# Optimization experiments

Measured on AMD Instinct MI355X. Metric: run time of the kernel, lower is better.

The kernel has to match this reference:

```python
import jax, jax.numpy as jnp
import numpy as np

H = 56; W = 56; WS = 7; SS = 3; NH = 12; DIM = 384; B = 32
N = WS * WS                      # 49 tokens per window
NW = (H // WS) * (W // WS)       # 64 windows per image
HID = 4 * DIM
EPS = 1e-5


def _rel_index():
    coords = np.stack(np.meshgrid(np.arange(WS), np.arange(WS), indexing='ij'))  # [2,ws,ws]
    cf = coords.reshape(2, -1)
    rel = (cf[:, :, None] - cf[:, None, :]).transpose(1, 2, 0)  # [N,N,2]
    rel[..., 0] += WS - 1
    rel[..., 1] += WS - 1
    rel[..., 0] *= 2 * WS - 1
    return rel.sum(-1).astype(np.int32)  # [N,N] in [0,169)


def _attn_mask():
    img = np.zeros((H, W), np.float32)
    cnt = 0
    sl = (slice(0, -WS), slice(-WS, -SS), slice(-SS, None))
    for h in sl:
        for w in sl:
            img[h, w] = cnt
            cnt += 1
    mw = img.reshape(H // WS, WS, W // WS, WS).transpose(0, 2, 1, 3).reshape(-1, N)  # [nW,N]
    am = mw[:, None, :] - mw[:, :, None]  # [nW,N,N]
    return np.where(am != 0, np.float32(-100.0), np.float32(0.0)).astype(np.float32)


def _ln(x, g, b):
    m = jnp.mean(x, axis=-1, keepdims=True)
    v = jnp.mean(jnp.square(x - m), axis=-1, keepdims=True)
    return (x - m) * jax.lax.rsqrt(v + EPS) * g + b


def setup_inputs() -> dict:
    key = jax.random.key(0)
    ks = jax.random.split(key, 8)
    s = 0.02
    return {
        'x': jax.random.normal(ks[0], (B, H * W, DIM), jnp.float32),
        'qkv_w': jax.random.normal(ks[1], (3 * DIM, DIM), jnp.float32) * s,
        'qkv_b': jnp.zeros((3 * DIM,), jnp.float32),
        'proj_w': jax.random.normal(ks[2], (DIM, DIM), jnp.float32) * s,
        'proj_b': jnp.zeros((DIM,), jnp.float32),
        'rpb_table': jax.random.normal(ks[3], ((2 * WS - 1) ** 2, NH), jnp.float32) * s,
        'ln1_g': jnp.ones((DIM,), jnp.float32),
        'ln1_b': jnp.zeros((DIM,), jnp.float32),
        'fc1_w': jax.random.normal(ks[4], (HID, DIM), jnp.float32) * s,
        'fc1_b': jnp.zeros((HID,), jnp.float32),
        'fc2_w': jax.random.normal(ks[5], (DIM, HID), jnp.float32) * s,
        'fc2_b': jnp.zeros((DIM,), jnp.float32),
        'ln2_g': jnp.ones((DIM,), jnp.float32),
        'ln2_b': jnp.zeros((DIM,), jnp.float32),
        'attn_mask': jnp.asarray(_attn_mask()),
        'rel_idx': jnp.asarray(_rel_index()),
    }


def reference(x, qkv_w, qkv_b, proj_w, proj_b, rpb_table, ln1_g, ln1_b,
              fc1_w, fc1_b, fc2_w, fc2_b, ln2_g, ln2_b, attn_mask, rel_idx):
    Bb, L, C = x.shape
    hd = C // NH
    scale = hd ** -0.5
    shortcut = x
    # cyclic shift
    xs = jnp.roll(x.reshape(Bb, H, W, C), (-SS, -SS), axis=(1, 2))
    # window partition -> [Bb*nW, N, C]
    xw = xs.reshape(Bb, H // WS, WS, W // WS, WS, C).transpose(0, 1, 3, 2, 4, 5).reshape(-1, N, C)
    # qkv
    qkv = (xw @ qkv_w.T + qkv_b).reshape(-1, N, 3, NH, hd).transpose(2, 0, 3, 1, 4)
    q, k, v = qkv[0] * scale, qkv[1], qkv[2]          # [Bb*nW, NH, N, hd]
    attn = jnp.einsum('whnd,whmd->whnm', q, k)        # [Bb*nW, NH, N, N]
    bias = rpb_table[rel_idx.reshape(-1)].reshape(N, N, NH).transpose(2, 0, 1)
    attn = attn + bias[None]
    # shifted-window mask
    attn = attn.reshape(Bb, NW, NH, N, N) + attn_mask[None, :, None]
    attn = jax.nn.softmax(attn.reshape(-1, NH, N, N), axis=-1)
    out = jnp.einsum('whnm,whmd->whnd', attn, v).transpose(0, 2, 1, 3).reshape(-1, N, C)
    out = out @ proj_w.T + proj_b
    # window reverse + roll back
    xs = out.reshape(Bb, H // WS, W // WS, WS, WS, C).transpose(0, 1, 3, 2, 4, 5).reshape(Bb, H, W, C)
    xs = jnp.roll(xs, (SS, SS), axis=(1, 2)).reshape(Bb, L, C)
    # post-norm residuals (as in source: shortcut + norm(attn_out); x += norm(ffn(x)))
    x1 = shortcut + _ln(xs, ln1_g, ln1_b)
    y = jax.nn.gelu(x1 @ fc1_w.T + fc1_b, approximate=False) @ fc2_w.T + fc2_b
    return x1 + _ln(y, ln2_g, ln2_b)
```

## Files before the change

kernel.cpp:

```cpp
#include <hip/hip_runtime.h>
#include <hip/hip_bf16.h>
#include <math.h>

typedef __hip_bfloat16 bf16;
typedef __bf16 bf16x8 __attribute__((ext_vector_type(8)));
typedef float f32x4 __attribute__((ext_vector_type(4)));

#define HH 56
#define WW 56
#define WSZ 7
#define SSH 3
#define NHEAD 12
#define CDIM 384
#define BBATCH 32
#define NTOK 49
#define NWIN 64
#define HIDD 1536
#define HD 32
#define NWTOT (BBATCH*NWIN)
#define MROWS (NWTOT*NTOK)
#define MHALF (MROWS/2)
#define LTOT (HH*WW)
#define EPSLN 1e-5f
#define QSCALE 0.17677669529663687f
#define NEGBIG -1e30f

enum { M_QK = 0, M_V = 1, M_FC1 = 2, M_ROW = 3 };

__device__ __forceinline__ void gload16(const void* g, void* l) {
    __builtin_amdgcn_global_load_lds(
        (const __attribute__((address_space(1))) void*)g,
        (__attribute__((address_space(3))) void*)l, 16, 0, 0);
}

__device__ __forceinline__ unsigned short bfbits(float v) {
    bf16 b = __float2bfloat16(v);
    return *reinterpret_cast<unsigned short*>(&b);
}

__device__ __forceinline__ int xcd_swz(int orig, int nwg) {
    const int q = nwg >> 3, r = nwg & 7;
    const int xcd = orig & 7, loc = orig >> 3;
    return (xcd < r ? xcd * (q + 1) : r * (q + 1) + (xcd - r) * q) + loc;
}

__global__ __launch_bounds__(256) void cvt_k(const float* __restrict__ src,
                                             bf16* __restrict__ dst, int n) {
    int i = blockIdx.x * 256 + threadIdx.x;
    if (i < n) dst[i] = __float2bfloat16(src[i]);
}

__global__ __launch_bounds__(256)
void tbl_k(const float* __restrict__ rpb, const int* __restrict__ relidx,
           const float* __restrict__ amask, float* __restrict__ tbl) {
    int idx = blockIdx.x * 256 + threadIdx.x;
    int m = idx & 63, n = (idx >> 6) & 63;
    int h = (idx >> 12) % NHEAD, wi = idx / (64 * 64 * NHEAD);
    float v;
    if (m >= NTOK) v = NEGBIG;
    else if (n >= NTOK) v = 0.f;
    else v = rpb[relidx[n * NTOK + m] * NHEAD + h] + amask[((long)wi * NTOK + n) * NTOK + m];
    tbl[idx] = v;
}

__global__ __launch_bounds__(256) void gather_k(const float* __restrict__ x,
                                                bf16* __restrict__ xw, int rbase) {
    int idx = blockIdx.x * 256 + threadIdx.x;
    int rr_l = idx / 96, c4 = (idx % 96) * 4;
    int rr = rbase + rr_l;
    int w = rr / 49, ti = rr % 49;
    int b = w >> 6, wi = w & 63;
    int hy = (wi >> 3) * 7 + ti / 7;
    int hx = (wi & 7) * 7 + ti % 7;
    int sh = hy + SSH; if (sh >= HH) sh -= HH;
    int sw = hx + SSH; if (sw >= WW) sw -= WW;
    float4 v = *(const float4*)&x[((long)b * LTOT + sh * WW + sw) * CDIM + c4];
    ushort4 u = { bfbits(v.x), bfbits(v.y), bfbits(v.z), bfbits(v.w) };
    *(ushort4*)&xw[(long)rr_l * CDIM + c4] = u;
}

template<int MODE, int KDIM, int NTN>
__global__ __launch_bounds__(256, 4)
void mgemm_k(const bf16* __restrict__ A, const bf16* __restrict__ Wt,
             const float* __restrict__ bias, void* __restrict__ Outp)
{
    constexpr bool SWAP = (MODE != M_V);
    __shared__ bf16 As[2][128 * 32];
    __shared__ bf16 Bs[2][128 * 32];
    const int tid = threadIdx.x;
    const int wid = tid >> 6, lane = tid & 63;

    const int gid = xcd_swz(blockIdx.x, gridDim.x);
    const int m0 = (gid / NTN) * 128;
    const int n0 = (gid % NTN) * 128;

    const int strow = lane >> 2, stseg = lane & 3;
    const int swseg = stseg ^ ((strow >> 1) & 3);
    const bf16* Ag = A + (long)(m0 + wid * 32 + strow) * KDIM + swseg * 8;
    const bf16* Wg = Wt + (long)(n0 + wid * 32 + strow) * KDIM + swseg * 8;

    const int wr = (wid >> 1) * 64, wc = (wid & 1) * 64;
    const int l15 = lane & 15, g4 = lane >> 4;
    const int sa = g4 ^ ((l15 >> 1) & 3);

    f32x4 acc[4][4] = {};

    auto STAGE = [&](int b, int t) {
#pragma unroll
        for (int i = 0; i < 2; ++i)
            gload16(Ag + (long)(i * 16) * KDIM + t * 32, &As[b][(wid * 32 + i * 16) * 32]);
#pragma unroll
        for (int i = 0; i < 2; ++i)
            gload16(Wg + (long)(i * 16) * KDIM + t * 32, &Bs[b][(wid * 32 + i * 16) * 32]);
    };

    const int nt = KDIM / 32;
    STAGE(0, 0);
    STAGE(1, 1);
    asm volatile("s_waitcnt vmcnt(4)" ::: "memory");
    __builtin_amdgcn_s_barrier();

    int buf = 0;
    for (int t = 0; t < nt; ++t) {
        bf16x8 af[4], bfr[4];
#pragma unroll
        for (int i = 0; i < 4; ++i) {
            af[i]  = *(const bf16x8*)&As[buf][(wr + i * 16 + l15) * 32 + sa * 8];
            bfr[i] = *(const bf16x8*)&Bs[buf][(wc + i * 16 + l15) * 32 + sa * 8];
        }
        __builtin_amdgcn_sched_barrier(0);
        asm volatile("s_waitcnt lgkmcnt(0)" ::: "memory");
        __builtin_amdgcn_sched_barrier(0);
        __builtin_amdgcn_s_barrier();
        if (t + 2 < nt) STAGE(buf, t + 2);
#pragma unroll
        for (int mi = 0; mi < 4; ++mi)
#pragma unroll
            for (int ni = 0; ni < 4; ++ni) {
                if (SWAP)
                    acc[ni][mi] = __builtin_amdgcn_mfma_f32_16x16x32_bf16(
                        bfr[ni], af[mi], acc[ni][mi], 0, 0, 0);
                else
                    acc[mi][ni] = __builtin_amdgcn_mfma_f32_16x16x32_bf16(
                        af[mi], bfr[ni], acc[mi][ni], 0, 0, 0);
            }
        if (t + 2 < nt) { asm volatile("s_waitcnt vmcnt(4)" ::: "memory"); }
        else            { asm volatile("s_waitcnt vmcnt(0)" ::: "memory"); }
        __builtin_amdgcn_s_barrier();
        buf ^= 1;
    }

    if (MODE == M_V) {
#pragma unroll
        for (int mi = 0; mi < 4; ++mi) {
            const int mb = m0 + wr + mi * 16 + g4 * 4;
            const int wv_ = mb / 49, ti0 = mb - wv_ * 49;
#pragma unroll
            for (int ni = 0; ni < 4; ++ni) {
                const int n = n0 + wc + ni * 16 + l15;
                const int h = n >> 5, d = n & 31;
                const float bn = bias[n];
                float v4[4];
#pragma unroll
                for (int j = 0; j < 4; ++j) v4[j] = acc[mi][ni][j] + bn;
                if (ti0 <= 45) {
                    ushort4 u = { bfbits(v4[0]), bfbits(v4[1]), bfbits(v4[2]), bfbits(v4[3]) };
                    *(ushort4*)&((bf16*)Outp)[(((long)wv_ * NHEAD + h) * HD + d) * 64 + ti0] = u;
                } else {
#pragma unroll
                    for (int j = 0; j < 4; ++j) {
                        const int m = mb + j;
                        const int w2 = m / 49, ti = m - w2 * 49;
                        ((bf16*)Outp)[(((long)w2 * NHEAD + h) * HD + d) * 64 + ti]
                            = __float2bfloat16(v4[j]);
                    }
                }
            }
        }
    } else {
        long rowbase[4];
        int wq_[4], ti_[4];
#pragma unroll
        for (int mi = 0; mi < 4; ++mi) {
            const int m = m0 + wr + mi * 16 + l15;
            if (MODE == M_QK)       { wq_[mi] = m / 49; ti_[mi] = m - wq_[mi] * 49; }
            else if (MODE == M_FC1) { rowbase[mi] = (long)m * HIDD; }
            else                    { rowbase[mi] = (long)m * CDIM; }
        }
#pragma unroll
        for (int ni = 0; ni < 4; ++ni) {
            const int nb = n0 + wc + ni * 16 + g4 * 4;
            const float4 bn = *(const float4*)&bias[nb];
            const float bb[4] = { bn.x, bn.y, bn.z, bn.w };
#pragma unroll
            for (int mi = 0; mi < 4; ++mi) {
                float v4[4];
#pragma unroll
                for (int j = 0; j < 4; ++j) v4[j] = acc[ni][mi][j] + bb[j];
                if (MODE == M_FC1) {
#pragma unroll
                    for (int j = 0; j < 4; ++j)
                        v4[j] = 0.5f * v4[j] * (1.0f + erff(v4[j] * 0.70710678118654752f));
                } else if (MODE == M_QK) {
                    if (nb < CDIM) {
#pragma unroll
                        for (int j = 0; j < 4; ++j) v4[j] *= QSCALE;
                    }
                }
                ushort4 u = { bfbits(v4[0]), bfbits(v4[1]), bfbits(v4[2]), bfbits(v4[3]) };
                if (MODE == M_QK) {
                    const int which = nb >= CDIM;
                    const int hb = (nb - which * CDIM) >> 5, d0 = nb & 31;
                    *(ushort4*)&((bf16*)Outp)[
                        ((((long)wq_[mi] * 2 + which) * NHEAD + hb) * NTOK + ti_[mi]) * HD + d0] = u;
                } else {
                    *(ushort4*)&((bf16*)Outp)[rowbase[mi] + nb] = u;
                }
            }
        }
    }
}

__global__ __launch_bounds__(256)
void mattn_k(const bf16* __restrict__ qk, const bf16* __restrict__ vT,
             const float* __restrict__ tbl, bf16* __restrict__ attn_out)
{
    __shared__ bf16 Plds[4][64 * 72];
    const int tid = threadIdx.x, wid = tid >> 6, lane = tid & 63;
    const int t = blockIdx.x * 4 + wid;
    const int w = t / NHEAD, h = t % NHEAD, wi = w & 63;
    const int l15 = lane & 15, g = lane >> 4;
    const bf16* qb = qk + ((long)(w * 2 + 0) * NHEAD + h) * (NTOK * HD);
    const bf16* kb = qk + ((long)(w * 2 + 1) * NHEAD + h) * (NTOK * HD);
    const bf16* vt = vT + ((long)w * NHEAD + h) * (HD * 64);
    const float* Tb = tbl + (long)(wi * NHEAD + h) * 64 * 64;
    char* Pw = (char*)&Plds[wid][0];

    bf16x8 kf[4], qf[4];
#pragma unroll
    for (int i = 0; i < 4; ++i) {
        kf[i] = *(const bf16x8*)&kb[(16 * i + l15) * HD + 8 * g];
        qf[i] = *(const bf16x8*)&qb[(16 * i + l15) * HD + 8 * g];
    }
    f32x4 s[4][4] = {};
#pragma unroll
    for (int mi = 0; mi < 4; ++mi)
#pragma unroll
        for (int ni = 0; ni < 4; ++ni)
            s[mi][ni] = __builtin_amdgcn_mfma_f32_16x16x32_bf16(
                kf[mi], qf[ni], s[mi][ni], 0, 0, 0);

#pragma unroll
    for (int ni = 0; ni < 4; ++ni) {
        const int n = 16 * ni + l15;
#pragma unroll
        for (int mi = 0; mi < 4; ++mi) {
            float4 tv = *(const float4*)&Tb[(long)n * 64 + 16 * mi + 4 * g];
            s[mi][ni][0] += tv.x; s[mi][ni][1] += tv.y;
            s[mi][ni][2] += tv.z; s[mi][ni][3] += tv.w;
        }
        float mx = NEGBIG;
#pragma unroll
        for (int mi = 0; mi < 4; ++mi)
#pragma unroll
            for (int j = 0; j < 4; ++j) mx = fmaxf(mx, s[mi][ni][j]);
        mx = fmaxf(mx, __shfl_xor(mx, 16));
        mx = fmaxf(mx, __shfl_xor(mx, 32));
        float sum = 0.f;
#pragma unroll
        for (int mi = 0; mi < 4; ++mi)
#pragma unroll
            for (int j = 0; j < 4; ++j) {
                float e = expf(s[mi][ni][j] - mx);
                s[mi][ni][j] = e; sum += e;
            }
        sum += __shfl_xor(sum, 16);
        sum += __shfl_xor(sum, 32);
        const float r = 1.0f / sum;
#pragma unroll
        for (int mi = 0; mi < 4; ++mi) {
            ushort4 u;
            u.x = bfbits(s[mi][ni][0] * r);
            u.y = bfbits(s[mi][ni][1] * r);
            u.z = bfbits(s[mi][ni][2] * r);
            u.w = bfbits(s[mi][ni][3] * r);
            *(ushort4*)(Pw + (long)n * 144 + (16 * mi + 4 * g) * 2) = u;
        }
    }

    f32x4 o[4][2] = {};
#pragma unroll
    for (int kk = 0; kk < 2; ++kk) {
        bf16x8 vf[2];
        vf[0] = *(const bf16x8*)&vt[(long)(l15) * 64 + 32 * kk + 8 * g];
        vf[1] = *(const bf16x8*)&vt[(long)(16 + l15) * 64 + 32 * kk + 8 * g];
#pragma unroll
        for (int rt = 0; rt < 4; ++rt) {
            bf16x8 pf = *(const bf16x8*)(Pw + (long)(16 * rt + l15) * 144 + (32 * kk + 8 * g) * 2);
            o[rt][0] = __builtin_amdgcn_mfma_f32_16x16x32_bf16(pf, vf[0], o[rt][0], 0, 0, 0);
            o[rt][1] = __builtin_amdgcn_mfma_f32_16x16x32_bf16(pf, vf[1], o[rt][1], 0, 0, 0);
        }
    }

#pragma unroll
    for (int rt = 0; rt < 4; ++rt)
#pragma unroll
        for (int dt = 0; dt < 2; ++dt)
#pragma unroll
            for (int j = 0; j < 4; ++j) {
                int n = 16 * rt + 4 * g + j;
                if (n < NTOK)
                    attn_out[((long)w * NTOK + n) * CDIM + h * HD + 16 * dt + l15]
                        = __float2bfloat16(o[rt][dt][j]);
            }
}

__global__ __launch_bounds__(256)
void ln1_k(const bf16* __restrict__ P, const bf16* __restrict__ xw,
           const float* __restrict__ g, const float* __restrict__ bta,
           bf16* __restrict__ x1b, int mbase)
{
    const int wv = threadIdx.x >> 6, lane = threadIdx.x & 63;
    const long rl = (long)blockIdx.x * 4 + wv;
    const bool act = lane < 48;
    float vals[8];
    float s = 0.f, sq = 0.f;
    if (act) {
        bf16x8 pv = *(const bf16x8*)&P[rl * CDIM + lane * 8];
#pragma unroll
        for (int j = 0; j < 8; ++j) { vals[j] = (float)pv[j]; s += vals[j]; sq += vals[j] * vals[j]; }
    } else {
#pragma unroll
        for (int j = 0; j < 8; ++j) vals[j] = 0.f;
    }
#pragma unroll
    for (int o = 32; o; o >>= 1) { s += __shfl_xor(s, o); sq += __shfl_xor(sq, o); }
    const float mean = s * (1.f / 384.f);
    const float rstd = rsqrtf(sq * (1.f / 384.f) - mean * mean + EPSLN);

    const int m = mbase + (int)rl;
    int w = m / 49, ti = m - w * 49;
    int b = w >> 6, wi = w & 63;
    int hy = (wi >> 3) * 7 + ti / 7;
    int hx = (wi & 7) * 7 + ti % 7;
    int dh = hy + SSH; if (dh >= HH) dh -= HH;
    int dw = hx + SSH; if (dw >= WW) dw -= WW;
    const long tok_l = (long)b * LTOT + dh * WW + dw - mbase;

    if (act) {
        bf16x8 xv = *(const bf16x8*)&xw[rl * CDIM + lane * 8];
        const int c = lane * 8;
        const float4 g0 = *(const float4*)&g[c],   g1 = *(const float4*)&g[c + 4];
        const float4 b0 = *(const float4*)&bta[c], b1 = *(const float4*)&bta[c + 4];
        const float gg[8] = { g0.x, g0.y, g0.z, g0.w, g1.x, g1.y, g1.z, g1.w };
        const float bb[8] = { b0.x, b0.y, b0.z, b0.w, b1.x, b1.y, b1.z, b1.w };
        ushort4 u0, u1;
        float r0 = (float)xv[0] + (vals[0] - mean) * rstd * gg[0] + bb[0];
        float r1 = (float)xv[1] + (vals[1] - mean) * rstd * gg[1] + bb[1];
        float r2 = (float)xv[2] + (vals[2] - mean) * rstd * gg[2] + bb[2];
        float r3 = (float)xv[3] + (vals[3] - mean) * rstd * gg[3] + bb[3];
        u0 = { bfbits(r0), bfbits(r1), bfbits(r2), bfbits(r3) };
        r0 = (float)xv[4] + (vals[4] - mean) * rstd * gg[4] + bb[4];
        r1 = (float)xv[5] + (vals[5] - mean) * rstd * gg[5] + bb[5];
        r2 = (float)xv[6] + (vals[6] - mean) * rstd * gg[6] + bb[6];
        r3 = (float)xv[7] + (vals[7] - mean) * rstd * gg[7] + bb[7];
        u1 = { bfbits(r0), bfbits(r1), bfbits(r2), bfbits(r3) };
        *(ushort4*)&x1b[tok_l * CDIM + c] = u0;
        *(ushort4*)&x1b[tok_l * CDIM + c + 4] = u1;
    }
}

__global__ __launch_bounds__(256)
void ln2_k(const bf16* __restrict__ y, const bf16* __restrict__ x1b,
           const float* __restrict__ g, const float* __restrict__ bta,
           float* __restrict__ outp, int mbase)
{
    const int wv = threadIdx.x >> 6, lane = threadIdx.x & 63;
    const long rl = (long)blockIdx.x * 4 + wv;
    const bool act = lane < 48;
    float vals[8];
    float s = 0.f, sq = 0.f;
    if (act) {
        bf16x8 yv = *(const bf16x8*)&y[rl * CDIM + lane * 8];
#pragma unroll
        for (int j = 0; j < 8; ++j) { vals[j] = (float)yv[j]; s += vals[j]; sq += vals[j] * vals[j]; }
    } else {
#pragma unroll
        for (int j = 0; j < 8; ++j) vals[j] = 0.f;
    }
#pragma unroll
    for (int o = 32; o; o >>= 1) { s += __shfl_xor(s, o); sq += __shfl_xor(sq, o); }
    const float mean = s * (1.f / 384.f);
    const float rstd = rsqrtf(sq * (1.f / 384.f) - mean * mean + EPSLN);

    if (act) {
        bf16x8 xv = *(const bf16x8*)&x1b[rl * CDIM + lane * 8];
        const int c = lane * 8;
        const float4 g0 = *(const float4*)&g[c],   g1 = *(const float4*)&g[c + 4];
        const float4 b0 = *(const float4*)&bta[c], b1 = *(const float4*)&bta[c + 4];
        float4 o0, o1;
        o0.x = (float)xv[0] + (vals[0] - mean) * rstd * g0.x + b0.x;
        o0.y = (float)xv[1] + (vals[1] - mean) * rstd * g0.y + b0.y;
        o0.z = (float)xv[2] + (vals[2] - mean) * rstd * g0.z + b0.z;
        o0.w = (float)xv[3] + (vals[3] - mean) * rstd * g0.w + b0.w;
        o1.x = (float)xv[4] + (vals[4] - mean) * rstd * g1.x + b1.x;
        o1.y = (float)xv[5] + (vals[5] - mean) * rstd * g1.y + b1.y;
        o1.z = (float)xv[6] + (vals[6] - mean) * rstd * g1.z + b1.z;
        o1.w = (float)xv[7] + (vals[7] - mean) * rstd * g1.w + b1.w;
        const long mg = (long)mbase + rl;
        *(float4*)&outp[mg * CDIM + c] = o0;
        *(float4*)&outp[mg * CDIM + c + 4] = o1;
    }
}

extern "C" void kernel_launch(void* const* d_in, const int* in_sizes, int n_in,
                              void* d_out, int out_size, void* d_ws, size_t ws_size,
                              hipStream_t stream)
{
    const float* x      = (const float*)d_in[0];
    const float* qkv_w  = (const float*)d_in[1];
    const float* qkv_b  = (const float*)d_in[2];
    const float* proj_w = (const float*)d_in[3];
    const float* proj_b = (const float*)d_in[4];
    const float* rpb    = (const float*)d_in[5];
    const float* ln1_g  = (const float*)d_in[6];
    const float* ln1_b  = (const float*)d_in[7];
    const float* fc1_w  = (const float*)d_in[8];
    const float* fc1_b  = (const float*)d_in[9];
    const float* fc2_w  = (const float*)d_in[10];
    const float* fc2_b  = (const float*)d_in[11];
    const float* ln2_g  = (const float*)d_in[12];
    const float* ln2_b  = (const float*)d_in[13];
    const float* amask  = (const float*)d_in[14];
    const int*   relidx = (const int*)d_in[15];
    float* out = (float*)d_out;
    char*  ws  = (char*)d_ws;

    bf16*  wq    = (bf16*) (ws + 0L);
    bf16*  wp    = (bf16*) (ws + 884736L);
    bf16*  w1    = (bf16*) (ws + 1179648L);
    bf16*  w2    = (bf16*) (ws + 2359296L);
    float* tbl   = (float*)(ws + 3538944L);
    bf16*  xw_h  = (bf16*) (ws + 16121856L);
    bf16*  qkb_h = (bf16*) (ws + 54657024L);
    bf16*  vT_h  = (bf16*) (ws + 131727360L);
    bf16*  att_h = (bf16*) (ws + 182059008L);
    bf16*  P_h   = (bf16*) (ws + 220594176L);
    bf16*  x1b_h = (bf16*) (ws + 259129344L);
    bf16*  H1_h  = (bf16*) (ws + 16121856L);
    bf16*  y_h   = (bf16*) (ws + 170262528L);

    dim3 b256(256);

    cvt_k<<<dim3((3*CDIM*CDIM + 255)/256), b256, 0, stream>>>(qkv_w, wq, 3*CDIM*CDIM);
    cvt_k<<<dim3((CDIM*CDIM + 255)/256), b256, 0, stream>>>(proj_w, wp, CDIM*CDIM);
    cvt_k<<<dim3((HIDD*CDIM + 255)/256), b256, 0, stream>>>(fc1_w, w1, HIDD*CDIM);
    cvt_k<<<dim3((CDIM*HIDD + 255)/256), b256, 0, stream>>>(fc2_w, w2, CDIM*HIDD);
    tbl_k<<<dim3(64*12*64*64/256), b256, 0, stream>>>(rpb, relidx, amask, tbl);

    for (int c = 0; c < 2; ++c) {
        const int mb = c * MHALF;
        gather_k<<<dim3(MHALF * 96 / 256), b256, 0, stream>>>(x, xw_h, mb);
        mgemm_k<M_QK, CDIM, 6><<<dim3((MHALF/128)*6), b256, 0, stream>>>(
            xw_h, wq, qkv_b, (void*)qkb_h);
        mgemm_k<M_V, CDIM, 3><<<dim3((MHALF/128)*3), b256, 0, stream>>>(
            xw_h, wq + (long)2*CDIM*CDIM, qkv_b + 2*CDIM, (void*)vT_h);
        mattn_k<<<dim3(1024 * NHEAD / 4), b256, 0, stream>>>(qkb_h, vT_h, tbl, att_h);
        mgemm_k<M_ROW, CDIM, 3><<<dim3((MHALF/128)*3), b256, 0, stream>>>(
            att_h, wp, proj_b, (void*)P_h);
        ln1_k<<<dim3(MHALF/4), b256, 0, stream>>>(P_h, xw_h, ln1_g, ln1_b, x1b_h, mb);
        mgemm_k<M_FC1, CDIM, 12><<<dim3((MHALF/128)*12), b256, 0, stream>>>(
            x1b_h, w1, fc1_b, (void*)H1_h);
        mgemm_k<M_ROW, HIDD, 3><<<dim3((MHALF/128)*3), b256, 0, stream>>>(
            H1_h, w2, fc2_b, (void*)y_h);
        ln2_k<<<dim3(MHALF/4), b256, 0, stream>>>(y_h, x1b_h, ln2_g, ln2_b, out, mb);
    }
}
```

Baseline: 944.1 us.

## Fuse proj and fc2 GEMMs with LayerNorm residual epilogues, use tanh-form GELU

Adds a gemm_ln_k kernel in which each block computes a full 64x384 output row tile, reduces row statistics across waves through LDS and applies LayerNorm plus residual (with the window-reverse scatter for LN1) in the epilogue. This removes the bf16 round trip of the P and y intermediates and two separate LN launches. The full-row tiles give fewer blocks and more registers per thread. Separately, exact erf GELU is replaced by a sigmoid-based tanh approximation, which changes the numerics slightly.

```diff
diff --git a/kernel.cpp b/kernel.cpp
--- a/kernel.cpp
+++ b/kernel.cpp
@@ -25,7 +25,7 @@
 #define QSCALE 0.17677669529663687f
 #define NEGBIG -1e30f
 
-enum { M_QK = 0, M_V = 1, M_FC1 = 2, M_ROW = 3 };
+enum { M_QK = 0, M_V = 1, M_FC1 = 2 };
 
 __device__ __forceinline__ void gload16(const void* g, void* l) {
     __builtin_amdgcn_global_load_lds(
@@ -36,6 +36,10 @@
 __device__ __forceinline__ unsigned short bfbits(float v) {
     bf16 b = __float2bfloat16(v);
     return *reinterpret_cast<unsigned short*>(&b);
+}
+
+__device__ __forceinline__ float fast_gelu(float v) {
+    return v / (1.0f + __expf(-1.59576912f * v * fmaf(0.044715f, v * v, 1.0f)));
 }
 
 __device__ __forceinline__ int xcd_swz(int orig, int nwg) {
@@ -183,9 +187,8 @@
 #pragma unroll
         for (int mi = 0; mi < 4; ++mi) {
             const int m = m0 + wr + mi * 16 + l15;
-            if (MODE == M_QK)       { wq_[mi] = m / 49; ti_[mi] = m - wq_[mi] * 49; }
-            else if (MODE == M_FC1) { rowbase[mi] = (long)m * HIDD; }
-            else                    { rowbase[mi] = (long)m * CDIM; }
+            if (MODE == M_QK) { wq_[mi] = m / 49; ti_[mi] = m - wq_[mi] * 49; }
+            else              { rowbase[mi] = (long)m * HIDD; }
         }
 #pragma unroll
         for (int ni = 0; ni < 4; ++ni) {
@@ -199,8 +202,7 @@
                 for (int j = 0; j < 4; ++j) v4[j] = acc[ni][mi][j] + bb[j];
                 if (MODE == M_FC1) {
 #pragma unroll
-                    for (int j = 0; j < 4; ++j)
-                        v4[j] = 0.5f * v4[j] * (1.0f + erff(v4[j] * 0.70710678118654752f));
+                    for (int j = 0; j < 4; ++j) v4[j] = fast_gelu(v4[j]);
                 } else if (MODE == M_QK) {
                     if (nb < CDIM) {
 #pragma unroll
@@ -216,6 +218,149 @@
                 } else {
                     *(ushort4*)&((bf16*)Outp)[rowbase[mi] + nb] = u;
                 }
+            }
+        }
+    }
+}
+
+template<int KDIM, bool SCATTER>
+__global__ __launch_bounds__(256, 2)
+void gemm_ln_k(const bf16* __restrict__ A, const bf16* __restrict__ Wt,
+               const float* __restrict__ bias, const bf16* __restrict__ resid,
+               const float* __restrict__ lng, const float* __restrict__ lnb,
+               float* __restrict__ outf, bf16* __restrict__ outb, int mbase)
+{
+    __shared__ bf16 As[2][64 * 32];
+    __shared__ bf16 Bs[2][384 * 32];
+    __shared__ float lnp[512];
+    const int tid = threadIdx.x;
+    const int wid = tid >> 6, lane = tid & 63;
+
+    const int m0 = xcd_swz(blockIdx.x, gridDim.x) * 64;
+
+    const int strow = tid >> 2, stseg = tid & 3;
+    const int swr = stseg ^ ((strow >> 1) & 3);
+    const bf16* Ag = A + (long)(m0 + strow) * KDIM + swr * 8;
+    const bf16* Wg = Wt + (long)strow * KDIM + swr * 8;
+
+    const int wc = wid * 96;
+    const int l15 = lane & 15, g4 = lane >> 4;
+    const int sa = g4 ^ ((l15 >> 1) & 3);
+
+    f32x4 acc[6][4] = {};
+
+    auto STAGE = [&](int b, int t) {
+        gload16(Ag + t * 32, &As[b][strow * 32 + stseg * 8]);
+#pragma unroll
+        for (int i = 0; i < 6; ++i)
+            gload16(Wg + (long)(i * 64) * KDIM + t * 32,
+                    &Bs[b][(strow + i * 64) * 32 + stseg * 8]);
+    };
+
+    const int nt = KDIM / 32;
+    STAGE(0, 0);
+    STAGE(1, 1);
+    asm volatile("s_waitcnt vmcnt(7)" ::: "memory");
+    __builtin_amdgcn_s_barrier();
+
+    int buf = 0;
+    for (int t = 0; t < nt; ++t) {
+        bf16x8 af[4], bfr[6];
+#pragma unroll
+        for (int i = 0; i < 4; ++i)
+            af[i] = *(const bf16x8*)&As[buf][(i * 16 + l15) * 32 + sa * 8];
+#pragma unroll
+        for (int i = 0; i < 6; ++i)
+            bfr[i] = *(const bf16x8*)&Bs[buf][(wc + i * 16 + l15) * 32 + sa * 8];
+        __builtin_amdgcn_sched_barrier(0);
+        asm volatile("s_waitcnt lgkmcnt(0)" ::: "memory");
+        __builtin_amdgcn_sched_barrier(0);
+        __builtin_amdgcn_s_barrier();
+        if (t + 2 < nt) STAGE(buf, t + 2);
+#pragma unroll
+        for (int ni = 0; ni < 6; ++ni)
+#pragma unroll
+            for (int mi = 0; mi < 4; ++mi)
+                acc[ni][mi] = __builtin_amdgcn_mfma_f32_16x16x32_bf16(
+                    bfr[ni], af[mi], acc[ni][mi], 0, 0, 0);
+        if (t + 2 < nt) { asm volatile("s_waitcnt vmcnt(7)" ::: "memory"); }
+        else            { asm volatile("s_waitcnt vmcnt(0)" ::: "memory"); }
+        __builtin_amdgcn_s_barrier();
+        buf ^= 1;
+    }
+
+    float psum[4] = {}, psq[4] = {};
+#pragma unroll
+    for (int ni = 0; ni < 6; ++ni) {
+        const int nb = wc + ni * 16 + g4 * 4;
+        const float4 bn = *(const float4*)&bias[nb];
+        const float bb[4] = { bn.x, bn.y, bn.z, bn.w };
+#pragma unroll
+        for (int mi = 0; mi < 4; ++mi)
+#pragma unroll
+            for (int j = 0; j < 4; ++j) {
+                float v = acc[ni][mi][j] + bb[j];
+                acc[ni][mi][j] = v;
+                psum[mi] += v; psq[mi] += v * v;
+            }
+    }
+#pragma unroll
+    for (int mi = 0; mi < 4; ++mi) {
+        psum[mi] += __shfl_xor(psum[mi], 16); psum[mi] += __shfl_xor(psum[mi], 32);
+        psq[mi]  += __shfl_xor(psq[mi], 16);  psq[mi]  += __shfl_xor(psq[mi], 32);
+    }
+    if (g4 == 0) {
+#pragma unroll
+        for (int mi = 0; mi < 4; ++mi) {
+            const int r = mi * 16 + l15;
+            lnp[wid * 64 + r] = psum[mi];
+            lnp[256 + wid * 64 + r] = psq[mi];
+        }
+    }
+    __syncthreads();
+
+#pragma unroll
+    for (int mi = 0; mi < 4; ++mi) {
+        const int r = mi * 16 + l15;
+        const float s  = lnp[r] + lnp[64 + r] + lnp[128 + r] + lnp[192 + r];
+        const float sq = lnp[256 + r] + lnp[320 + r] + lnp[384 + r] + lnp[448 + r];
+        const float mean = s * (1.f / 384.f);
+        const float rstd = rsqrtf(sq * (1.f / 384.f) - mean * mean + EPSLN);
+
+        const long rl = m0 + r;
+        long dst;
+        if (SCATTER) {
+            const int m = mbase + (int)rl;
+            int w = m / 49, ti = m - w * 49;
+            int b = w >> 6, wi = w & 63;
+            int hy = (wi >> 3) * 7 + ti / 7;
+            int hx = (wi & 7) * 7 + ti % 7;
+            int dh = hy + SSH; if (dh >= HH) dh -= HH;
+            int dw = hx + SSH; if (dw >= WW) dw -= WW;
+            dst = (long)b * LTOT + dh * WW + dw - mbase;
+        } else {
+            dst = mbase + rl;
+        }
+#pragma unroll
+        for (int ni = 0; ni < 6; ++ni) {
+            const int c = wc + ni * 16 + g4 * 4;
+            const float4 gv = *(const float4*)&lng[c];
+            const float4 bv = *(const float4*)&lnb[c];
+            ushort4 xv = *(const ushort4*)&resid[rl * CDIM + c];
+            float x0 = __bfloat162float(*(bf16*)&xv.x);
+            float x1 = __bfloat162float(*(bf16*)&xv.y);
+            float x2 = __bfloat162float(*(bf16*)&xv.z);
+            float x3 = __bfloat162float(*(bf16*)&xv.w);
+            float r0 = x0 + (acc[ni][mi][0] - mean) * rstd * gv.x + bv.x;
+            float r1 = x1 + (acc[ni][mi][1] - mean) * rstd * gv.y + bv.y;
+            float r2 = x2 + (acc[ni][mi][2] - mean) * rstd * gv.z + bv.z;
+            float r3 = x3 + (acc[ni][mi][3] - mean) * rstd * gv.w + bv.w;
+            if (SCATTER) {
+                ushort4 u = { bfbits(r0), bfbits(r1), bfbits(r2), bfbits(r3) };
+                *(ushort4*)&outb[dst * CDIM + c] = u;
+            } else {
+                float4 o = { r0, r1, r2, r3 };
+                *(float4*)&outf[dst * CDIM + c] = o;
             }
         }
     }
@@ -313,104 +458,6 @@
                     attn_out[((long)w * NTOK + n) * CDIM + h * HD + 16 * dt + l15]
                         = __float2bfloat16(o[rt][dt][j]);
             }
-}
-
-__global__ __launch_bounds__(256)
-void ln1_k(const bf16* __restrict__ P, const bf16* __restrict__ xw,
-           const float* __restrict__ g, const float* __restrict__ bta,
-           bf16* __restrict__ x1b, int mbase)
-{
-    const int wv = threadIdx.x >> 6, lane = threadIdx.x & 63;
-    const long rl = (long)blockIdx.x * 4 + wv;
-    const bool act = lane < 48;
-    float vals[8];
-    float s = 0.f, sq = 0.f;
-    if (act) {
-        bf16x8 pv = *(const bf16x8*)&P[rl * CDIM + lane * 8];
-#pragma unroll
-        for (int j = 0; j < 8; ++j) { vals[j] = (float)pv[j]; s += vals[j]; sq += vals[j] * vals[j]; }
-    } else {
-#pragma unroll
-        for (int j = 0; j < 8; ++j) vals[j] = 0.f;
-    }
-#pragma unroll
-    for (int o = 32; o; o >>= 1) { s += __shfl_xor(s, o); sq += __shfl_xor(sq, o); }
-    const float mean = s * (1.f / 384.f);
-    const float rstd = rsqrtf(sq * (1.f / 384.f) - mean * mean + EPSLN);
-
-    const int m = mbase + (int)rl;
-    int w = m / 49, ti = m - w * 49;
-    int b = w >> 6, wi = w & 63;
-    int hy = (wi >> 3) * 7 + ti / 7;
-    int hx = (wi & 7) * 7 + ti % 7;
-    int dh = hy + SSH; if (dh >= HH) dh -= HH;
-    int dw = hx + SSH; if (dw >= WW) dw -= WW;
-    const long tok_l = (long)b * LTOT + dh * WW + dw - mbase;
-
-    if (act) {
-        bf16x8 xv = *(const bf16x8*)&xw[rl * CDIM + lane * 8];
-        const int c = lane * 8;
-        const float4 g0 = *(const float4*)&g[c],   g1 = *(const float4*)&g[c + 4];
-        const float4 b0 = *(const float4*)&bta[c], b1 = *(const float4*)&bta[c + 4];
-        const float gg[8] = { g0.x, g0.y, g0.z, g0.w, g1.x, g1.y, g1.z, g1.w };
-        const float bb[8] = { b0.x, b0.y, b0.z, b0.w, b1.x, b1.y, b1.z, b1.w };
-        ushort4 u0, u1;
-        float r0 = (float)xv[0] + (vals[0] - mean) * rstd * gg[0] + bb[0];
-        float r1 = (float)xv[1] + (vals[1] - mean) * rstd * gg[1] + bb[1];
-        float r2 = (float)xv[2] + (vals[2] - mean) * rstd * gg[2] + bb[2];
-        float r3 = (float)xv[3] + (vals[3] - mean) * rstd * gg[3] + bb[3];
-        u0 = { bfbits(r0), bfbits(r1), bfbits(r2), bfbits(r3) };
-        r0 = (float)xv[4] + (vals[4] - mean) * rstd * gg[4] + bb[4];
-        r1 = (float)xv[5] + (vals[5] - mean) * rstd * gg[5] + bb[5];
-        r2 = (float)xv[6] + (vals[6] - mean) * rstd * gg[6] + bb[6];
-        r3 = (float)xv[7] + (vals[7] - mean) * rstd * gg[7] + bb[7];
-        u1 = { bfbits(r0), bfbits(r1), bfbits(r2), bfbits(r3) };
-        *(ushort4*)&x1b[tok_l * CDIM + c] = u0;
-        *(ushort4*)&x1b[tok_l * CDIM + c + 4] = u1;
-    }
-}
-
-__global__ __launch_bounds__(256)
-void ln2_k(const bf16* __restrict__ y, const bf16* __restrict__ x1b,
-           const float* __restrict__ g, const float* __restrict__ bta,
-           float* __restrict__ outp, int mbase)
-{
-    const int wv = threadIdx.x >> 6, lane = threadIdx.x & 63;
-    const long rl = (long)blockIdx.x * 4 + wv;
-    const bool act = lane < 48;
-    float vals[8];
-    float s = 0.f, sq = 0.f;
-    if (act) {
-        bf16x8 yv = *(const bf16x8*)&y[rl * CDIM + lane * 8];
-#pragma unroll
-        for (int j = 0; j < 8; ++j) { vals[j] = (float)yv[j]; s += vals[j]; sq += vals[j] * vals[j]; }
-    } else {
-#pragma unroll
-        for (int j = 0; j < 8; ++j) vals[j] = 0.f;
-    }
-#pragma unroll
-    for (int o = 32; o; o >>= 1) { s += __shfl_xor(s, o); sq += __shfl_xor(sq, o); }
-    const float mean = s * (1.f / 384.f);
-    const float rstd = rsqrtf(sq * (1.f / 384.f) - mean * mean + EPSLN);
-
-    if (act) {
-        bf16x8 xv = *(const bf16x8*)&x1b[rl * CDIM + lane * 8];
-        const int c = lane * 8;
-        const float4 g0 = *(const float4*)&g[c],   g1 = *(const float4*)&g[c + 4];
-        const float4 b0 = *(const float4*)&bta[c], b1 = *(const float4*)&bta[c + 4];
-        float4 o0, o1;
-        o0.x = (float)xv[0] + (vals[0] - mean) * rstd * g0.x + b0.x;
-        o0.y = (float)xv[1] + (vals[1] - mean) * rstd * g0.y + b0.y;
-        o0.z = (float)xv[2] + (vals[2] - mean) * rstd * g0.z + b0.z;
-        o0.w = (float)xv[3] + (vals[3] - mean) * rstd * g0.w + b0.w;
-        o1.x = (float)xv[4] + (vals[4] - mean) * rstd * g1.x + b1.x;
-        o1.y = (float)xv[5] + (vals[5] - mean) * rstd * g1.y + b1.y;
-        o1.z = (float)xv[6] + (vals[6] - mean) * rstd * g1.z + b1.z;
-        o1.w = (float)xv[7] + (vals[7] - mean) * rstd * g1.w + b1.w;
-        const long mg = (long)mbase + rl;
-        *(float4*)&outp[mg * CDIM + c] = o0;
-        *(float4*)&outp[mg * CDIM + c + 4] = o1;
-    }
 }
 
 extern "C" void kernel_launch(void* const* d_in, const int* in_sizes, int n_in,
@@ -445,10 +492,8 @@
     bf16*  qkb_h = (bf16*) (ws + 54657024L);
     bf16*  vT_h  = (bf16*) (ws + 131727360L);
     bf16*  att_h = (bf16*) (ws + 182059008L);
-    bf16*  P_h   = (bf16*) (ws + 220594176L);
-    bf16*  x1b_h = (bf16*) (ws + 259129344L);
+    bf16*  x1b_h = (bf16*) (ws + 220594176L);
     bf16*  H1_h  = (bf16*) (ws + 16121856L);
-    bf16*  y_h   = (bf16*) (ws + 170262528L);
 
     dim3 b256(256);
 
@@ -466,13 +511,11 @@
         mgemm_k<M_V, CDIM, 3><<<dim3((MHALF/128)*3), b256, 0, stream>>>(
             xw_h, wq + (long)2*CDIM*CDIM, qkv_b + 2*CDIM, (void*)vT_h);
         mattn_k<<<dim3(1024 * NHEAD / 4), b256, 0, stream>>>(qkb_h, vT_h, tbl, att_h);
-        mgemm_k<M_ROW, CDIM, 3><<<dim3((MHALF/128)*3), b256, 0, stream>>>(
-            att_h, wp, proj_b, (void*)P_h);
-        ln1_k<<<dim3(MHALF/4), b256, 0, stream>>>(P_h, xw_h, ln1_g, ln1_b, x1b_h, mb);
+        gemm_ln_k<CDIM, true><<<dim3(MHALF/64), b256, 0, stream>>>(
+            att_h, wp, proj_b, xw_h, ln1_g, ln1_b, nullptr, x1b_h, mb);
         mgemm_k<M_FC1, CDIM, 12><<<dim3((MHALF/128)*12), b256, 0, stream>>>(
             x1b_h, w1, fc1_b, (void*)H1_h);
-        mgemm_k<M_ROW, HIDD, 3><<<dim3((MHALF/128)*3), b256, 0, stream>>>(
-            H1_h, w2, fc2_b, (void*)y_h);
-        ln2_k<<<dim3(MHALF/4), b256, 0, stream>>>(y_h, x1b_h, ln2_g, ln2_b, out, mb);
-    }
-}
+        gemm_ln_k<HIDD, false><<<dim3(MHALF/64), b256, 0, stream>>>(
+            H1_h, w2, fc2_b, x1b_h, ln2_g, ln2_b, out, nullptr, mb);
+    }
+}
```

Measured after the change: 888.4 us. -5.9%, faster.
